# Optimization experiments

Measured on AMD Instinct MI355X. Metric: run time of the kernel, lower is better.

Reference implementation:

```python
import jax, jax.numpy as jnp
import numpy as np

DIM = 180
HEADS = 6
WIN = 12
NGS = 2304          # num_gs_seed -> gs len
SQ = 48             # sqrt(num_gs_seed)
B = 64              # window-batch
TABLE = (2 * max(SQ, WIN) - 1) ** 2  # 9025 rows in bias table


def _rel_pos_index():
    # Mirrors the torch __init__ buffer construction (np.unique gives the
    # deterministic sorted-unique indexing the original intends).
    cs = (np.indices((SQ, SQ)) + 0.5) * WIN          # [2, SQ, SQ]
    ct = (np.indices((WIN, WIN)) + 0.5) * SQ
    d = cs.reshape(2, -1)[:, :, None] - ct.reshape(2, -1)[:, None, :]
    _, inv = np.unique(d.flatten(), return_inverse=True)
    idx = inv.reshape(d.shape).astype(np.int64)
    idx[0] *= idx.max()
    return jnp.asarray(idx.sum(0), dtype=jnp.int32)


def setup_inputs() -> dict:
    key = jax.random.key(0)
    ks = jax.random.split(key, 12)
    std = 0.02
    d = DIM
    inp = {
        "gs": jax.random.normal(ks[0], (B, NGS, d), dtype=jnp.float32),
        "feat": jax.random.normal(ks[1], (B, WIN * WIN, d), dtype=jnp.float32),
        "Wq": jax.random.normal(ks[2], (d, d), dtype=jnp.float32) * std,
        "bq": jnp.zeros((d,), dtype=jnp.float32),
        "Wk": jax.random.normal(ks[3], (d, d), dtype=jnp.float32) * std,
        "bk": jnp.zeros((d,), dtype=jnp.float32),
        "Wv": jax.random.normal(ks[4], (d, d), dtype=jnp.float32) * std,
        "bv": jnp.zeros((d,), dtype=jnp.float32),
        "Wp": jax.random.normal(ks[5], (d, d), dtype=jnp.float32) * std,
        "bp": jnp.zeros((d,), dtype=jnp.float32),
        "bias_table": jax.random.normal(ks[6], (TABLE, HEADS), dtype=jnp.float32) * std,
        "rel_pos_index": _rel_pos_index(),
    }
    return inp


def reference(gs, feat, Wq, bq, Wk, bk, Wv, bv, Wp, bp, bias_table, rel_pos_index):
    b, ng, c = gs.shape
    n = feat.shape[1]
    hd = c // HEADS
    scale = hd ** (-0.5)

    q = (gs @ Wq + bq).reshape(b, ng, HEADS, hd).transpose(0, 2, 1, 3) * scale  # [b,H,ng,hd]
    k = (feat @ Wk + bk).reshape(b, n, HEADS, hd).transpose(0, 2, 1, 3)          # [b,H,n,hd]
    v = (feat @ Wv + bv).reshape(b, n, HEADS, hd).transpose(0, 2, 1, 3)

    attn = jnp.einsum('bhqd,bhkd->bhqk', q, k)                                    # [b,H,ng,n]
    bias = bias_table[rel_pos_index]                                              # [ng,n,H]
    attn = attn + jnp.transpose(bias, (2, 0, 1))[None]                            # broadcast over b
    attn = jax.nn.softmax(attn, axis=-1)

    x = jnp.einsum('bhqk,bhkd->bhqd', attn, v)                                    # [b,H,ng,hd]
    x = x.transpose(0, 2, 1, 3).reshape(b, ng, c)
    return x @ Wp + bp
```

## Files before the change

kernel.cpp:

```cpp
#include <hip/hip_runtime.h>

#define DIM   180
#define HEADS 6
#define HD    30
#define NKEY  144
#define NGS   2304
#define BATCH 64
#define TQ    64
#define QT    36
#define WPAD  192
#define SXS   200
#define SPS   152
#define KROW  40
#define VROW  144
#define KB_STRIDE (NKEY * KROW)
#define VB_STRIDE (32 * VROW)

typedef unsigned short u16;
typedef short v8s __attribute__((ext_vector_type(8)));
typedef float v4f __attribute__((ext_vector_type(4)));

__device__ __forceinline__ float bf2f(u16 u) {
    union { unsigned int i; float f; } w; w.i = ((unsigned int)u) << 16; return w.f;
}
__device__ __forceinline__ u16 f2bf(float f) {
    union { float f; unsigned int i; } w; w.f = f;
    unsigned int r = w.i + 0x7fffu + ((w.i >> 16) & 1u);
    return (u16)(r >> 16);
}
__device__ __forceinline__ uint2 pack4(const v4f& x) {
    uint2 r;
    r.x = (unsigned)f2bf(x[0]) | ((unsigned)f2bf(x[1]) << 16);
    r.y = (unsigned)f2bf(x[2]) | ((unsigned)f2bf(x[3]) << 16);
    return r;
}

__global__ __launch_bounds__(256) void wt_prep_kernel(
    const float* __restrict__ Wq, const float* __restrict__ Wp,
    u16* __restrict__ WqT, u16* __restrict__ WpT) {
    int idx = blockIdx.x * 256 + threadIdx.x;
    int sel = idx >= WPAD * WPAD;
    int rr  = sel ? idx - WPAD * WPAD : idx;
    int j = rr / WPAD, k = rr - j * WPAD;
    float v;
    if (!sel) {
        v = (j < DIM && k < DIM) ? Wq[k * DIM + j] : 0.f;
        WqT[j * WPAD + k] = f2bf(v);
    } else {
        int h = k >> 5, dd = k & 31;
        v = (j < DIM && dd < HD) ? Wp[(h * HD + dd) * DIM + j] : 0.f;
        WpT[j * WPAD + k] = f2bf(v);
    }
}

__global__ __launch_bounds__(256) void gather_bias_kernel(
    const float* __restrict__ table, const int* __restrict__ rpi,
    u16* __restrict__ biasCT) {
    int i = blockIdx.x * 256 + threadIdx.x;
    int lane = i & 63;
    int tile = i >> 6;
    int t = tile % 9;
    int rem = tile / 9;
    int g = rem % 144;
    int h = rem / 144;
    int q  = 16 * g + (lane & 15);
    int n0 = 16 * t + (lane >> 4) * 4;
    const int4 rr = *(const int4*)&rpi[q * NKEY + n0];
    unsigned lo = (unsigned)f2bf(table[rr.x * HEADS + h]) |
                  ((unsigned)f2bf(table[rr.y * HEADS + h]) << 16);
    unsigned hi = (unsigned)f2bf(table[rr.z * HEADS + h]) |
                  ((unsigned)f2bf(table[rr.w * HEADS + h]) << 16);
    ((uint2*)biasCT)[i] = make_uint2(lo, hi);
}

__global__ __launch_bounds__(256) void kv_proj_kernel(
    const float* __restrict__ feat,
    const float* __restrict__ Wk, const float* __restrict__ bk,
    const float* __restrict__ Wv, const float* __restrict__ bv,
    u16* __restrict__ Kb, u16* __restrict__ VbT) {
    __shared__ float sF[16 * DIM];
    int b  = blockIdx.x / 9;
    int n0 = (blockIdx.x % 9) * 16;
    int tid = threadIdx.x;
    {
        const float4* src = (const float4*)(feat + (size_t)(b * NKEY + n0) * DIM);
        float4* dst = (float4*)sF;
        for (int i = tid; i < 16 * 45; i += 256) dst[i] = src[i];
    }
    __syncthreads();
    int j = tid;
    if (j < DIM) {
        float ak[16], av[16];
#pragma unroll
        for (int r = 0; r < 16; ++r) { ak[r] = 0.f; av[r] = 0.f; }
        const float4* sF4 = (const float4*)sF;
        for (int kc = 0; kc < 45; ++kc) {
            int kk = kc * 4;
            float wk0 = Wk[(kk + 0) * DIM + j], wk1 = Wk[(kk + 1) * DIM + j];
            float wk2 = Wk[(kk + 2) * DIM + j], wk3 = Wk[(kk + 3) * DIM + j];
            float wv0 = Wv[(kk + 0) * DIM + j], wv1 = Wv[(kk + 1) * DIM + j];
            float wv2 = Wv[(kk + 2) * DIM + j], wv3 = Wv[(kk + 3) * DIM + j];
#pragma unroll
            for (int r = 0; r < 16; ++r) {
                float4 g = sF4[r * 45 + kc];
                ak[r] = fmaf(g.x, wk0, ak[r]); ak[r] = fmaf(g.y, wk1, ak[r]);
                ak[r] = fmaf(g.z, wk2, ak[r]); ak[r] = fmaf(g.w, wk3, ak[r]);
                av[r] = fmaf(g.x, wv0, av[r]); av[r] = fmaf(g.y, wv1, av[r]);
                av[r] = fmaf(g.z, wv2, av[r]); av[r] = fmaf(g.w, wv3, av[r]);
            }
        }
        int h = j / HD, d = j - HD * h;
        u16* kp = Kb  + (size_t)(b * HEADS + h) * KB_STRIDE;
        u16* vp = VbT + (size_t)(b * HEADS + h) * VB_STRIDE;
        float bkj = bk[j], bvj = bv[j];
#pragma unroll
        for (int r = 0; r < 16; ++r) {
            kp[(n0 + r) * KROW + d] = f2bf(ak[r] + bkj);
            vp[d * VROW + n0 + r]   = f2bf(av[r] + bvj);
        }
    }
}

__global__ __launch_bounds__(256, 3) void attn_kernel(
    const float* __restrict__ gs,
    const u16* __restrict__ WqT, const float* __restrict__ bq,
    const u16* __restrict__ WpT, const float* __restrict__ bp,
    const u16* __restrict__ Kb, const u16* __restrict__ VbT,
    const u16* __restrict__ biasCT, float* __restrict__ out) {

    __shared__ u16 sXQ[TQ * SXS];
    __shared__ u16 sP[TQ * SPS];

    const int tid  = threadIdx.x;
    const int w    = tid >> 6;
    const int lane = tid & 63;
    const int l15  = tid & 15;
    const int quad = (tid >> 4) & 3;
    const int b    = blockIdx.x / QT;
    const int qt   = blockIdx.x % QT;
    const int q0   = qt * TQ;
    const float SCALE = 0.18257418583505536f;

    {
        const float4* src = (const float4*)(gs + (size_t)(b * NGS + q0) * DIM);
        for (int i = tid; i < TQ * 45; i += 256) {
            int row = i / 45, c = i - row * 45;
            float4 g = src[row * 45 + c];
            unsigned lo = (unsigned)f2bf(g.x) | ((unsigned)f2bf(g.y) << 16);
            unsigned hi = (unsigned)f2bf(g.z) | ((unsigned)f2bf(g.w) << 16);
            *(uint2*)&sXQ[row * SXS + c * 4] = make_uint2(lo, hi);
        }
        for (int i = tid; i < TQ * 16; i += 256)
            sXQ[(i >> 4) * SXS + 180 + (i & 15)] = 0;
    }
    __syncthreads();

    v4f qacc[12];
#pragma unroll
    for (int i = 0; i < 12; ++i) qacc[i] = (v4f){0.f, 0.f, 0.f, 0.f};
    for (int kt = 0; kt < 6; ++kt) {
        v8s A[4];
#pragma unroll
        for (int m = 0; m < 4; ++m)
            A[m] = *(const v8s*)&sXQ[(16 * m + l15) * SXS + kt * 32 + quad * 8];
#pragma unroll
        for (int jj = 0; jj < 3; ++jj) {
            v8s B = *(const v8s*)&WqT[(size_t)((3 * w + jj) * 16 + l15) * WPAD +
                                      kt * 32 + quad * 8];
#pragma unroll
            for (int m = 0; m < 4; ++m)
                qacc[jj * 4 + m] = __builtin_amdgcn_mfma_f32_16x16x32_bf16(
                    A[m], B, qacc[jj * 4 + m], 0, 0, 0);
        }
    }
    __syncthreads();
#pragma unroll
    for (int jj = 0; jj < 3; ++jj) {
        int j = (3 * w + jj) * 16 + l15;
        if (j < DIM) {
            int h = j / HD;
            int pos = j + 2 * h;
            float bqj = bq[j];
#pragma unroll
            for (int m = 0; m < 4; ++m)
#pragma unroll
                for (int r = 0; r < 4; ++r)
                    sXQ[(16 * m + quad * 4 + r) * SXS + pos] =
                        f2bf((qacc[jj * 4 + m][r] + bqj) * SCALE);
        }
    }
    for (int i = tid; i < TQ * 12; i += 256) {
        int row = i / 12, c = i - row * 12;
        sXQ[row * SXS + (c >> 1) * 32 + 30 + (c & 1)] = 0;
    }
    __syncthreads();

    for (int h = 0; h < HEADS; ++h) {
        const u16* kp = Kb  + (size_t)(b * HEADS + h) * KB_STRIDE;
        const u16* vp = VbT + (size_t)(b * HEADS + h) * VB_STRIDE;

        v8s qa = *(const v8s*)&sXQ[(16 * w + l15) * SXS + h * 32 + quad * 8];

        v4f la[9];
        const u16* bgt = biasCT +
            ((size_t)((h * 144 + (qt * 4 + w)) * 9) * 256) + lane * 4;
#pragma unroll
        for (int t = 0; t < 9; ++t) {
            uint2 bb = *(const uint2*)(bgt + t * 256);
            v4f c;
            c[0] = bf2f((u16)(bb.x & 0xffff));
            c[1] = bf2f((u16)(bb.x >> 16));
            c[2] = bf2f((u16)(bb.y & 0xffff));
            c[3] = bf2f((u16)(bb.y >> 16));
            v8s kb = *(const v8s*)&kp[(16 * t + l15) * KROW + quad * 8];
            la[t] = __builtin_amdgcn_mfma_f32_16x16x32_bf16(kb, qa, c, 0, 0, 0);
        }

        float m = la[0][0];
#pragma unroll
        for (int t = 0; t < 9; ++t)
#pragma unroll
            for (int r = 0; r < 4; ++r) m = fmaxf(m, la[t][r]);
        m = fmaxf(m, __shfl_xor(m, 16));
        m = fmaxf(m, __shfl_xor(m, 32));
        float s = 0.f;
#pragma unroll
        for (int t = 0; t < 9; ++t)
#pragma unroll
            for (int r = 0; r < 4; ++r) {
                la[t][r] = __expf(la[t][r] - m);
                s += la[t][r];
            }
        s += __shfl_xor(s, 16);
        s += __shfl_xor(s, 32);
        float inv = 1.f / s;

#pragma unroll
        for (int t = 0; t < 9; ++t) {
            v4f p;
#pragma unroll
            for (int r = 0; r < 4; ++r) p[r] = la[t][r] * inv;
            *(uint2*)&sP[(16 * w + l15) * SPS + 16 * t + quad * 4] = pack4(p);
        }

        v4f x0 = (v4f){0.f, 0.f, 0.f, 0.f}, x1 = x0;
        for (int kt = 0; kt < 5; ++kt) {
            v8s pa = (v8s){0,0,0,0,0,0,0,0}, a0 = pa, a1 = pa;
            if (!(kt == 4 && quad >= 2)) {
                pa = *(const v8s*)&sP[(16 * w + l15) * SPS + kt * 32 + quad * 8];
                a0 = *(const v8s*)&vp[l15 * VROW + kt * 32 + quad * 8];
                a1 = *(const v8s*)&vp[(16 + l15) * VROW + kt * 32 + quad * 8];
            }
            x0 = __builtin_amdgcn_mfma_f32_16x16x32_bf16(a0, pa, x0, 0, 0, 0);
            x1 = __builtin_amdgcn_mfma_f32_16x16x32_bf16(a1, pa, x1, 0, 0, 0);
        }
        *(uint2*)&sXQ[(16 * w + l15) * SXS + h * 32 + quad * 4]      = pack4(x0);
        *(uint2*)&sXQ[(16 * w + l15) * SXS + h * 32 + 16 + quad * 4] = pack4(x1);
    }
    __syncthreads();

    {
        v4f acc[12];
#pragma unroll
        for (int i = 0; i < 12; ++i) acc[i] = (v4f){0.f, 0.f, 0.f, 0.f};
        for (int kt = 0; kt < 6; ++kt) {
            v8s A[4];
#pragma unroll
            for (int m = 0; m < 4; ++m)
                A[m] = *(const v8s*)&sXQ[(16 * m + l15) * SXS + kt * 32 + quad * 8];
#pragma unroll
            for (int jj = 0; jj < 3; ++jj) {
                v8s B = *(const v8s*)&WpT[(size_t)((3 * w + jj) * 16 + l15) * WPAD +
                                          kt * 32 + quad * 8];
#pragma unroll
                for (int m = 0; m < 4; ++m)
                    acc[jj * 4 + m] = __builtin_amdgcn_mfma_f32_16x16x32_bf16(
                        A[m], B, acc[jj * 4 + m], 0, 0, 0);
            }
        }
#pragma unroll
        for (int jj = 0; jj < 3; ++jj) {
            int j = (3 * w + jj) * 16 + l15;
            if (j < DIM) {
                float bpj = bp[j];
#pragma unroll
                for (int m = 0; m < 4; ++m)
#pragma unroll
                    for (int r = 0; r < 4; ++r)
                        out[(size_t)(b * NGS + q0 + 16 * m + quad * 4 + r) * DIM + j] =
                            acc[jj * 4 + m][r] + bpj;
            }
        }
    }
}

extern "C" void kernel_launch(void* const* d_in, const int* in_sizes, int n_in,
                              void* d_out, int out_size, void* d_ws, size_t ws_size,
                              hipStream_t stream) {
    const float* gs    = (const float*)d_in[0];
    const float* feat  = (const float*)d_in[1];
    const float* Wq    = (const float*)d_in[2];
    const float* bq    = (const float*)d_in[3];
    const float* Wk    = (const float*)d_in[4];
    const float* bk    = (const float*)d_in[5];
    const float* Wv    = (const float*)d_in[6];
    const float* bv    = (const float*)d_in[7];
    const float* Wp    = (const float*)d_in[8];
    const float* bp    = (const float*)d_in[9];
    const float* table = (const float*)d_in[10];
    const int*   rpi   = (const int*)d_in[11];
    float* out = (float*)d_out;

    u16* WqT    = (u16*)d_ws;
    u16* WpT    = WqT + WPAD * WPAD;
    u16* Kb     = WpT + WPAD * WPAD;
    u16* VbT    = Kb  + (size_t)BATCH * HEADS * KB_STRIDE;
    u16* biasCT = VbT + (size_t)BATCH * HEADS * VB_STRIDE;

    size_t zero_bytes = (size_t)BATCH * HEADS * (KB_STRIDE + VB_STRIDE) * sizeof(u16);
    hipMemsetAsync(Kb, 0, zero_bytes, stream);

    wt_prep_kernel<<<dim3(2 * WPAD * WPAD / 256), dim3(256), 0, stream>>>(Wq, Wp, WqT, WpT);
    gather_bias_kernel<<<dim3(HEADS * 144 * 9 * 64 / 256), dim3(256), 0, stream>>>(
        table, rpi, biasCT);
    kv_proj_kernel<<<dim3(BATCH * 9), dim3(256), 0, stream>>>(feat, Wk, bk, Wv, bv, Kb, VbT);
    attn_kernel<<<dim3(BATCH * QT), dim3(256), 0, stream>>>(
        gs, WqT, bq, WpT, bp, Kb, VbT, biasCT, out);
}
```

Before: 383.0 us.

## Keep softmax probabilities in registers via permlane32 swap instead of LDS staging

```diff
diff --git a/kernel.cpp b/kernel.cpp
--- a/kernel.cpp
+++ b/kernel.cpp
@@ -10,7 +10,6 @@
 #define QT    36
 #define WPAD  192
 #define SXS   200
-#define SPS   152
 #define KROW  40
 #define VROW  144
 #define KB_STRIDE (NKEY * KROW)
@@ -34,6 +33,7 @@
     r.y = (unsigned)f2bf(x[2]) | ((unsigned)f2bf(x[3]) << 16);
     return r;
 }
+
 
 __global__ __launch_bounds__(256) void wt_prep_kernel(
     const float* __restrict__ Wq, const float* __restrict__ Wp,
@@ -63,8 +63,10 @@
     int rem = tile / 9;
     int g = rem % 144;
     int h = rem / 144;
+    int qd = (lane >> 4) & 3;
+    int pg = ((qd & 1) << 1) | (qd >> 1);
     int q  = 16 * g + (lane & 15);
-    int n0 = 16 * t + (lane >> 4) * 4;
+    int n0 = 16 * t + pg * 4;
     const int4 rr = *(const int4*)&rpi[q * NKEY + n0];
     unsigned lo = (unsigned)f2bf(table[rr.x * HEADS + h]) |
                   ((unsigned)f2bf(table[rr.y * HEADS + h]) << 16);
@@ -115,13 +117,14 @@
         float bkj = bk[j], bvj = bv[j];
 #pragma unroll
         for (int r = 0; r < 16; ++r) {
-            kp[(n0 + r) * KROW + d] = f2bf(ak[r] + bkj);
-            vp[d * VROW + n0 + r]   = f2bf(av[r] + bvj);
-        }
-    }
-}
-
-__global__ __launch_bounds__(256, 3) void attn_kernel(
+            int sr = ((r >> 2) == 1) ? r + 4 : ((r >> 2) == 2) ? r - 4 : r;
+            kp[(n0 + sr) * KROW + d] = f2bf(ak[r] + bkj);
+            vp[d * VROW + n0 + r]    = f2bf(av[r] + bvj);
+        }
+    }
+}
+
+__global__ __launch_bounds__(256, 6) void attn_kernel(
     const float* __restrict__ gs,
     const u16* __restrict__ WqT, const float* __restrict__ bq,
     const u16* __restrict__ WpT, const float* __restrict__ bp,
@@ -129,7 +132,6 @@
     const u16* __restrict__ biasCT, float* __restrict__ out) {
 
     __shared__ u16 sXQ[TQ * SXS];
-    __shared__ u16 sP[TQ * SPS];
 
     const int tid  = threadIdx.x;
     const int w    = tid >> 6;
@@ -235,24 +237,35 @@
         s += __shfl_xor(s, 32);
         float inv = 1.f / s;
 
+        unsigned sd0[9], sd1[9];
 #pragma unroll
         for (int t = 0; t < 9; ++t) {
-            v4f p;
-#pragma unroll
-            for (int r = 0; r < 4; ++r) p[r] = la[t][r] * inv;
-            *(uint2*)&sP[(16 * w + l15) * SPS + 16 * t + quad * 4] = pack4(p);
+            sd0[t] = (unsigned)f2bf(la[t][0] * inv) |
+                     ((unsigned)f2bf(la[t][1] * inv) << 16);
+            sd1[t] = (unsigned)f2bf(la[t][2] * inv) |
+                     ((unsigned)f2bf(la[t][3] * inv) << 16);
         }
 
         v4f x0 = (v4f){0.f, 0.f, 0.f, 0.f}, x1 = x0;
+#pragma unroll
         for (int kt = 0; kt < 5; ++kt) {
-            v8s pa = (v8s){0,0,0,0,0,0,0,0}, a0 = pa, a1 = pa;
-            if (!(kt == 4 && quad >= 2)) {
-                pa = *(const v8s*)&sP[(16 * w + l15) * SPS + kt * 32 + quad * 8];
-                a0 = *(const v8s*)&vp[l15 * VROW + kt * 32 + quad * 8];
-                a1 = *(const v8s*)&vp[(16 + l15) * VROW + kt * 32 + quad * 8];
-            }
-            x0 = __builtin_amdgcn_mfma_f32_16x16x32_bf16(a0, pa, x0, 0, 0, 0);
-            x1 = __builtin_amdgcn_mfma_f32_16x16x32_bf16(a1, pa, x1, 0, 0, 0);
+            unsigned d0, d1, d2, d3;
+            if (kt < 4) {
+                d0 = sd0[2 * kt];     d1 = sd1[2 * kt];
+                d2 = sd0[2 * kt + 1]; d3 = sd1[2 * kt + 1];
+            } else {
+                d0 = sd0[8]; d1 = sd1[8]; d2 = 0u; d3 = 0u;
+            }
+            asm("v_permlane32_swap_b32 %0, %1" : "+v"(d0), "+v"(d2));
+            asm("v_permlane32_swap_b32 %0, %1" : "+v"(d1), "+v"(d3));
+            union { unsigned u[4]; v8s v; } pu;
+            pu.u[0] = d0; pu.u[1] = d1; pu.u[2] = d2; pu.u[3] = d3;
+            int co = kt * 32 + quad * 8;
+            co = (co < NKEY) ? co : 0;
+            v8s a0 = *(const v8s*)&vp[l15 * VROW + co];
+            v8s a1 = *(const v8s*)&vp[(16 + l15) * VROW + co];
+            x0 = __builtin_amdgcn_mfma_f32_16x16x32_bf16(a0, pu.v, x0, 0, 0, 0);
+            x1 = __builtin_amdgcn_mfma_f32_16x16x32_bf16(a1, pu.v, x1, 0, 0, 0);
         }
         *(uint2*)&sXQ[(16 * w + l15) * SXS + h * 32 + quad * 4]      = pack4(x0);
         *(uint2*)&sXQ[(16 * w + l15) * SXS + h * 32 + 16 + quad * 4] = pack4(x1);
```

New measurement: 436.2 us. 1.14x slower.
